# Kernel optimization log

Hardware: AMD Instinct MI355X
Metric: run time of the kernel (lower is better)

The kernel has to match this reference:

```python
import jax, jax.numpy as jnp
import numpy as np
import math

EPSILON = 1e-5
B, P, H, W = 64, 68, 64, 64


def setup_inputs() -> dict:
    key = jax.random.key(0)
    k1, k2, k3 = jax.random.split(key, 3)
    # probability heatmaps: positive, normalized over spatial dims
    hm = jax.random.uniform(k1, (B, P, H, W), dtype=jnp.float32) + 1e-3
    hm = hm / jnp.sum(hm, axis=(2, 3), keepdims=True)
    # means in pixel coordinates [0, W)
    means = jax.random.uniform(k2, (B, P, 2), dtype=jnp.float32) * (W - 1)
    # SPD 2x2 covariance, flattened to 4: Sigma = A A^T + c*I
    A = jax.random.normal(k3, (B, P, 2, 2), dtype=jnp.float32) * 2.0
    Sigma = jnp.einsum('bpij,bpkj->bpik', A, A) + 2.0 * jnp.eye(2, dtype=jnp.float32)
    covariance = Sigma.reshape(B, P, 4)
    return {"heatmaps": hm, "means": means, "covariance": covariance}


def reference(heatmaps, means, covariance):
    b, p, h, w = heatmaps.shape
    # grid: xv[i,j] = j, yv[i,j] = i
    yv, xv = jnp.meshgrid(jnp.arange(h, dtype=heatmaps.dtype),
                          jnp.arange(w, dtype=heatmaps.dtype), indexing='ij')
    Sigma = covariance.reshape(b, p, 2, 2)
    s00, s01 = Sigma[:, :, 0, 0], Sigma[:, :, 0, 1]
    s10, s11 = Sigma[:, :, 1, 0], Sigma[:, :, 1, 1]
    det = s00 * s11 - s01 * s10 + EPSILON                       # [b,p]
    # centered coordinates, [b,p,h,w]
    dx = xv[None, None] - means[:, :, 0, None, None]
    dy = yv[None, None] - means[:, :, 1, None, None]
    # quadratic form v^T Sigma^{-1} v with Sigma^{-1} = adj(Sigma)/det
    quad = (s11[..., None, None] * dx * dx
            - (s01 + s10)[..., None, None] * dx * dy
            + s00[..., None, None] * dy * dy) / det[..., None, None]
    log_prob_2 = -0.5 * quad
    prob = jnp.exp(log_prob_2) / (2.0 * math.pi * jnp.sqrt(det)[..., None, None])
    prob = prob / jnp.sum(prob, axis=(2, 3), keepdims=True)
    # KLDivLoss(reduce=False): target * (log target - input), target = heatmaps (detached)
    hm = heatmaps.reshape(b * p, h * w)
    pr = prob.reshape(b * p, h * w)
    kld = jax.scipy.special.xlogy(hm, hm) - hm * jnp.log(pr + EPSILON)
    loss = jnp.sum(kld, axis=1).mean()
    return loss
```

## Files before the change

kernel.cpp:

```cpp
#include <hip/hip_runtime.h>
#include <math.h>

#define EPS 1e-5f

constexpr int Bc = 64, Pc = 68, Hc = 64, Wc = 64;
constexpr int NPIX  = Hc * Wc;
constexpr int NTILE = Bc * Pc;
constexpr int BLK   = 256;
constexpr int PPT   = NPIX / BLK;

__device__ __forceinline__ float block_reduce_sum(float v, float* sbuf) {
    __syncthreads();
    #pragma unroll
    for (int o = 32; o > 0; o >>= 1) v += __shfl_down(v, o, 64);
    const int lane = threadIdx.x & 63;
    const int wid  = threadIdx.x >> 6;
    if (lane == 0) sbuf[wid] = v;
    __syncthreads();
    if (threadIdx.x == 0) {
        float s = sbuf[0] + sbuf[1] + sbuf[2] + sbuf[3];
        sbuf[4] = s;
    }
    __syncthreads();
    return sbuf[4];
}

__global__ __launch_bounds__(BLK)
void gauss_kld_tile_kernel(const float* __restrict__ hm,
                           const float* __restrict__ means,
                           const float* __restrict__ cov,
                           float* __restrict__ partial) {
    const int tile = blockIdx.x;
    const float* __restrict__ h = hm + (size_t)tile * NPIX;

    const float mx  = means[tile * 2 + 0];
    const float my  = means[tile * 2 + 1];
    const float s00 = cov[tile * 4 + 0];
    const float s01 = cov[tile * 4 + 1];
    const float s10 = cov[tile * 4 + 2];
    const float s11 = cov[tile * 4 + 3];
    const float det = s00 * s11 - s01 * s10 + EPS;
    const float inv_det = 1.0f / det;
    const float c_xx =  s11 * inv_det;
    const float c_xy = -(s01 + s10) * inv_det;
    const float c_yy =  s00 * inv_det;

    const int t = threadIdx.x;

    float lp[PPT];
    float hv[PPT];
    float esum = 0.0f;

    #pragma unroll
    for (int k = 0; k < PPT / 4; k++) {
        const int v = k * BLK + t;
        const float4 h4 = reinterpret_cast<const float4*>(h)[v];
        hv[k * 4 + 0] = h4.x;
        hv[k * 4 + 1] = h4.y;
        hv[k * 4 + 2] = h4.z;
        hv[k * 4 + 3] = h4.w;
        const int base = v * 4;
        #pragma unroll
        for (int c = 0; c < 4; c++) {
            const int idx = base + c;
            const float dy = (float)(idx >> 6) - my;
            const float dx = (float)(idx & 63) - mx;
            const float quad = c_xx * dx * dx + c_xy * dx * dy + c_yy * dy * dy;
            const float l = -0.5f * quad;
            lp[k * 4 + c] = l;
            esum += __expf(l);
        }
    }

    __shared__ float sbuf[8];
    const float S = block_reduce_sum(esum, sbuf);
    const float invS = 1.0f / S;

    float kl = 0.0f;
    #pragma unroll
    for (int i = 0; i < PPT; i++) {
        const float pr = __expf(lp[i]) * invS;
        const float hvi = hv[i];
        if (hvi > 0.0f) {
            kl += hvi * (__logf(hvi) - __logf(pr + EPS));
        } else {
            kl += -hvi * __logf(pr + EPS);
        }
    }

    const float tile_sum = block_reduce_sum(kl, sbuf);
    if (threadIdx.x == 0) partial[tile] = tile_sum;
}

__global__ __launch_bounds__(BLK)
void gauss_kld_reduce_kernel(const float* __restrict__ partial,
                             float* __restrict__ out) {
    float s = 0.0f;
    for (int i = threadIdx.x; i < NTILE; i += BLK) s += partial[i];
    __shared__ float sbuf[8];
    const float tot = block_reduce_sum(s, sbuf);
    if (threadIdx.x == 0) out[0] = tot / (float)NTILE;
}

extern "C" void kernel_launch(void* const* d_in, const int* in_sizes, int n_in,
                              void* d_out, int out_size, void* d_ws, size_t ws_size,
                              hipStream_t stream) {
    const float* hm    = (const float*)d_in[0];
    const float* means = (const float*)d_in[1];
    const float* cov   = (const float*)d_in[2];
    float* out = (float*)d_out;
    float* partial = (float*)d_ws;

    gauss_kld_tile_kernel<<<NTILE, BLK, 0, stream>>>(hm, means, cov, partial);
    gauss_kld_reduce_kernel<<<1, BLK, 0, stream>>>(partial, out);
}
```

Baseline: 107.4 us.

## Rewrite KL in log2 domain and fuse final reduction via atomics

Moves the Gaussian exponent into base-2 so a native exp2 can be used, and computes the quadratic incrementally per float4. The KL sum is split algebraically into sum h log h + ln S * sum h - sum h log(e + eps*S), which removes the per-pixel division and branch. The separate reduce kernel is replaced by slotted double atomics plus a last-block finish, with a tiny init kernel to zero the accumulators. This adds atomic traffic and a different floating-point summation order.

```diff
diff --git a/kernel.cpp b/kernel.cpp
--- a/kernel.cpp
+++ b/kernel.cpp
@@ -8,6 +8,10 @@
 constexpr int NTILE = Bc * Pc;
 constexpr int BLK   = 256;
 constexpr int PPT   = NPIX / BLK;
+constexpr int NSLOT = 64;
+
+constexpr float LOG2E = 1.44269504088896340736f;
+constexpr float LN2   = 0.69314718055994530942f;
 
 __device__ __forceinline__ float block_reduce_sum(float v, float* sbuf) {
     __syncthreads();
@@ -17,19 +21,25 @@
     const int wid  = threadIdx.x >> 6;
     if (lane == 0) sbuf[wid] = v;
     __syncthreads();
-    if (threadIdx.x == 0) {
-        float s = sbuf[0] + sbuf[1] + sbuf[2] + sbuf[3];
-        sbuf[4] = s;
-    }
+    if (threadIdx.x == 0) sbuf[4] = sbuf[0] + sbuf[1] + sbuf[2] + sbuf[3];
     __syncthreads();
     return sbuf[4];
 }
 
+__global__ __launch_bounds__(64)
+void init_kernel(double* __restrict__ acc, unsigned int* __restrict__ cnt) {
+    const int t = threadIdx.x;
+    if (t < NSLOT) acc[t] = 0.0;
+    if (t == 0)    *cnt  = 0u;
+}
+
 __global__ __launch_bounds__(BLK)
-void gauss_kld_tile_kernel(const float* __restrict__ hm,
-                           const float* __restrict__ means,
-                           const float* __restrict__ cov,
-                           float* __restrict__ partial) {
+void gauss_kld_fused_kernel(const float* __restrict__ hm,
+                            const float* __restrict__ means,
+                            const float* __restrict__ cov,
+                            double* __restrict__ acc,
+                            unsigned int* __restrict__ cnt,
+                            float* __restrict__ out) {
     const int tile = blockIdx.x;
     const float* __restrict__ h = hm + (size_t)tile * NPIX;
 
@@ -40,66 +50,69 @@
     const float s10 = cov[tile * 4 + 2];
     const float s11 = cov[tile * 4 + 3];
     const float det = s00 * s11 - s01 * s10 + EPS;
-    const float inv_det = 1.0f / det;
-    const float c_xx =  s11 * inv_det;
-    const float c_xy = -(s01 + s10) * inv_det;
-    const float c_yy =  s00 * inv_det;
+    const float kf  = -0.5f * LOG2E / det;
+    const float axx =  kf * s11;
+    const float axy = -kf * (s01 + s10);
+    const float ayy =  kf * s00;
 
     const int t = threadIdx.x;
 
-    float lp[PPT];
+    float ev[PPT];
     float hv[PPT];
-    float esum = 0.0f;
+    float esum = 0.0f, hlog = 0.0f, hsum = 0.0f;
 
     #pragma unroll
-    for (int k = 0; k < PPT / 4; k++) {
-        const int v = k * BLK + t;
+    for (int kk = 0; kk < PPT / 4; kk++) {
+        const int v = kk * BLK + t;
         const float4 h4 = reinterpret_cast<const float4*>(h)[v];
-        hv[k * 4 + 0] = h4.x;
-        hv[k * 4 + 1] = h4.y;
-        hv[k * 4 + 2] = h4.z;
-        hv[k * 4 + 3] = h4.w;
-        const int base = v * 4;
+        const float dy  = (float)(v >> 4) - my;
+        const float dx0 = (float)((v & 15) << 2) - mx;
+        const float txy = axy * dy;
+        const float tyy = ayy * dy * dy;
         #pragma unroll
         for (int c = 0; c < 4; c++) {
-            const int idx = base + c;
-            const float dy = (float)(idx >> 6) - my;
-            const float dx = (float)(idx & 63) - mx;
-            const float quad = c_xx * dx * dx + c_xy * dx * dy + c_yy * dy * dy;
-            const float l = -0.5f * quad;
-            lp[k * 4 + c] = l;
-            esum += __expf(l);
+            const float dx = dx0 + (float)c;
+            const float l2 = fmaf(fmaf(axx, dx, txy), dx, tyy);
+            const float e  = __builtin_amdgcn_exp2f(l2);
+            ev[kk * 4 + c] = e;
+            esum += e;
+        }
+        hv[kk * 4 + 0] = h4.x; hv[kk * 4 + 1] = h4.y;
+        hv[kk * 4 + 2] = h4.z; hv[kk * 4 + 3] = h4.w;
+        #pragma unroll
+        for (int c = 0; c < 4; c++) {
+            const float hh = hv[kk * 4 + c];
+            hsum += hh;
+            hlog = fmaf(hh, __builtin_amdgcn_logf(fmaxf(hh, 1e-38f)), hlog);
         }
     }
 
     __shared__ float sbuf[8];
-    const float S = block_reduce_sum(esum, sbuf);
-    const float invS = 1.0f / S;
+    const float S    = block_reduce_sum(esum, sbuf);
+    const float cadd = EPS * S;
+    const float lnS  = __builtin_amdgcn_logf(S) * LN2;
 
-    float kl = 0.0f;
+    float kb = 0.0f;
     #pragma unroll
     for (int i = 0; i < PPT; i++) {
-        const float pr = __expf(lp[i]) * invS;
-        const float hvi = hv[i];
-        if (hvi > 0.0f) {
-            kl += hvi * (__logf(hvi) - __logf(pr + EPS));
-        } else {
-            kl += -hvi * __logf(pr + EPS);
-        }
+        kb = fmaf(hv[i], __builtin_amdgcn_logf(ev[i] + cadd), kb);
     }
+    const float contrib   = fmaf(lnS, hsum, LN2 * (hlog - kb));
+    const float tile_sum  = block_reduce_sum(contrib, sbuf);
 
-    const float tile_sum = block_reduce_sum(kl, sbuf);
-    if (threadIdx.x == 0) partial[tile] = tile_sum;
-}
-
-__global__ __launch_bounds__(BLK)
-void gauss_kld_reduce_kernel(const float* __restrict__ partial,
-                             float* __restrict__ out) {
-    float s = 0.0f;
-    for (int i = threadIdx.x; i < NTILE; i += BLK) s += partial[i];
-    __shared__ float sbuf[8];
-    const float tot = block_reduce_sum(s, sbuf);
-    if (threadIdx.x == 0) out[0] = tot / (float)NTILE;
+    __shared__ int is_last;
+    if (threadIdx.x == 0) {
+        atomicAdd(&acc[tile & (NSLOT - 1)], (double)tile_sum);
+        __threadfence();
+        is_last = (atomicAdd(cnt, 1u) == (unsigned)(gridDim.x - 1)) ? 1 : 0;
+    }
+    __syncthreads();
+    if (is_last && threadIdx.x < 64) {
+        double v = atomicAdd(&acc[threadIdx.x], 0.0);
+        #pragma unroll
+        for (int o = 32; o > 0; o >>= 1) v += __shfl_down(v, o, 64);
+        if (threadIdx.x == 0) out[0] = (float)(v / (double)NTILE);
+    }
 }
 
 extern "C" void kernel_launch(void* const* d_in, const int* in_sizes, int n_in,
@@ -109,8 +122,10 @@
     const float* means = (const float*)d_in[1];
     const float* cov   = (const float*)d_in[2];
     float* out = (float*)d_out;
-    float* partial = (float*)d_ws;
 
-    gauss_kld_tile_kernel<<<NTILE, BLK, 0, stream>>>(hm, means, cov, partial);
-    gauss_kld_reduce_kernel<<<1, BLK, 0, stream>>>(partial, out);
+    double*       acc = (double*)d_ws;
+    unsigned int* cnt = (unsigned int*)((char*)d_ws + NSLOT * sizeof(double));
+
+    init_kernel<<<1, 64, 0, stream>>>(acc, cnt);
+    gauss_kld_fused_kernel<<<NTILE, BLK, 0, stream>>>(hm, means, cov, acc, cnt, out);
 }
```

Result: slower. 217.1 us (+102.1%).
